# Optimization experiments

Measured on AMD Instinct MI355X. Metric: run time of the kernel, lower is better.

Reference implementation:

```python
import jax, jax.numpy as jnp
import numpy as np


def setup_inputs() -> dict:
    key = jax.random.key(0)
    k1, k2 = jax.random.split(key)
    src_map = jax.random.normal(k1, (8, 256, 48, 48), dtype=jnp.float32)
    dst_map = jax.random.normal(k2, (8, 256, 48, 48), dtype=jnp.float32)
    return {"src_map": src_map, "dst_map": dst_map}


def reference(src_map, dst_map):
    # src_map: [B, C, H, W] -> flatten spatial to S = H*W
    B, C, H, W = src_map.shape
    src_flat = src_map.reshape(B, C, H * W)                 # [B, C, S]
    # L2-normalize along channel dim (torch.norm default: 2-norm, no eps)
    src = src_flat / jnp.linalg.norm(src_flat, axis=1, keepdims=True)
    dst = dst_map / jnp.linalg.norm(dst_map, axis=1, keepdims=True)  # [B, C, Y, X]
    # cosine correlation volume: for each src pixel s, dot with every dst pixel
    gcm = jnp.einsum('bcs,bcyx->bsyx', src, dst)            # [B, S, Y, X]
    # torch.max(gcm, 0) == ReLU clamp
    return jnp.maximum(gcm, 0.0)
```

## Files before the change

### kernel.cpp

```cpp
#include <hip/hip_runtime.h>
#include <hip/hip_bf16.h>

#define B_DIM 8
#define C_DIM 256
#define S_DIM 2304

typedef __attribute__((ext_vector_type(8))) short short8;
typedef __attribute__((ext_vector_type(4))) float floatx4;

__device__ __forceinline__ void gload_lds16(const __hip_bfloat16* g, __hip_bfloat16* l) {
    __builtin_amdgcn_global_load_lds(
        (__attribute__((address_space(1))) void*)(void*)(g),
        (__attribute__((address_space(3))) void*)(l), 16, 0, 0);
}

__global__ __launch_bounds__(256) void norm_transpose_kernel(
    const float* __restrict__ src, const float* __restrict__ dst,
    __hip_bfloat16* __restrict__ srcT, __hip_bfloat16* __restrict__ dstT) {
    const int s0 = blockIdx.x * 64;
    const int b  = blockIdx.y;
    const float* in = (blockIdx.z == 0 ? src : dst) + (size_t)b * C_DIM * S_DIM;
    __hip_bfloat16* out = (blockIdx.z == 0 ? srcT : dstT) + (size_t)b * S_DIM * C_DIM;

    __shared__ __align__(16) __hip_bfloat16 tile[64][C_DIM + 8];
    __shared__ float red[4][64];
    __shared__ float invn[64];

    const int t  = threadIdx.x;
    const int l  = t & 63;
    const int wv = t >> 6;

    float ss = 0.f;
#pragma unroll 8
    for (int c = wv; c < C_DIM; c += 4) {
        float v = in[(size_t)c * S_DIM + s0 + l];
        ss += v * v;
        tile[l][c] = __float2bfloat16(v);
    }
    red[wv][l] = ss;
    __syncthreads();
    if (t < 64) invn[t] = rsqrtf(red[0][t] + red[1][t] + red[2][t] + red[3][t]);
    __syncthreads();

#pragma unroll
    for (int it = 0; it < 8; ++it) {
        int idx  = it * 256 + t;
        int srow = idx >> 5;
        int c0   = (idx & 31) << 3;
        float inv = invn[srow];
        union { short8 v; __hip_bfloat16 h[8]; } u, o;
        u.v = *(const short8*)&tile[srow][c0];
#pragma unroll
        for (int j = 0; j < 8; ++j)
            o.h[j] = __float2bfloat16(__bfloat162float(u.h[j]) * inv);
        *(short8*)&out[(size_t)(s0 + srow) * C_DIM + c0] = o.v;
    }
}

__global__ __launch_bounds__(256) void gemm_relu_kernel(
    const __hip_bfloat16* __restrict__ At, const __hip_bfloat16* __restrict__ Bt,
    float* __restrict__ out) {
    const int b  = blockIdx.z;
    const int m0 = blockIdx.y * 128;
    const int n0 = blockIdx.x * 128;
    const __hip_bfloat16* A  = At + (size_t)b * S_DIM * C_DIM;
    const __hip_bfloat16* Bp = Bt + (size_t)b * S_DIM * C_DIM;

    __shared__ __align__(16) __hip_bfloat16 As[128 * 32];
    __shared__ __align__(16) __hip_bfloat16 Bs[128 * 32];

    const int t    = threadIdx.x;
    const int lane = t & 63;
    const int wv   = t >> 6;

    const int fm = lane & 15;
    const int kq = (lane >> 4) << 3;
    const int wr = (wv >> 1) << 6;
    const int wc = (wv & 1) << 6;

    const int ch0 = wv * 2;

    floatx4 acc[4][4] = {};

    for (int k0 = 0; k0 < C_DIM; k0 += 32) {
#pragma unroll
        for (int ci = 0; ci < 2; ++ci) {
            int ch  = ch0 + ci;
            int e   = ch * 512 + lane * 8;
            int row = e >> 5;
            int kc  = e & 31;
            gload_lds16(A  + (size_t)(m0 + row) * C_DIM + (k0 + kc), &As[ch * 512]);
            gload_lds16(Bp + (size_t)(n0 + row) * C_DIM + (k0 + kc), &Bs[ch * 512]);
        }
        __syncthreads();

        short8 af[4], bf[4];
#pragma unroll
        for (int i = 0; i < 4; ++i) {
            af[i] = *(const short8*)&As[(wr + i * 16 + fm) * 32 + kq];
            bf[i] = *(const short8*)&Bs[(wc + i * 16 + fm) * 32 + kq];
        }
#pragma unroll
        for (int i = 0; i < 4; ++i)
#pragma unroll
            for (int j = 0; j < 4; ++j)
                acc[i][j] = __builtin_amdgcn_mfma_f32_16x16x32_bf16(af[i], bf[j], acc[i][j], 0, 0, 0);
        __syncthreads();
    }

    float* Cp = out + (size_t)b * S_DIM * S_DIM;
    const int rq = (lane >> 4) << 2;
#pragma unroll
    for (int i = 0; i < 4; ++i) {
        int rbase = m0 + wr + i * 16 + rq;
#pragma unroll
        for (int j = 0; j < 4; ++j) {
            int col = n0 + wc + j * 16 + fm;
#pragma unroll
            for (int r = 0; r < 4; ++r)
                Cp[(size_t)(rbase + r) * S_DIM + col] = fmaxf(acc[i][j][r], 0.f);
        }
    }
}

extern "C" void kernel_launch(void* const* d_in, const int* in_sizes, int n_in,
                              void* d_out, int out_size, void* d_ws, size_t ws_size,
                              hipStream_t stream) {
    const float* src = (const float*)d_in[0];
    const float* dst = (const float*)d_in[1];
    float* out = (float*)d_out;

    __hip_bfloat16* srcT = (__hip_bfloat16*)d_ws;
    __hip_bfloat16* dstT = srcT + (size_t)B_DIM * S_DIM * C_DIM;

    dim3 g1(S_DIM / 64, B_DIM, 2);
    norm_transpose_kernel<<<g1, 256, 0, stream>>>(src, dst, srcT, dstT);

    dim3 g2(S_DIM / 128, S_DIM / 128, B_DIM);
    gemm_relu_kernel<<<g2, 256, 0, stream>>>(srcT, dstT, out);
}
```

Before: 220.5 us.

## Double-buffer GEMM LDS tiles and stage epilogue through LDS for vector stores

The GEMM K-loop now double-buffers the A/B tiles in shared memory, prefetching the next K slice with global_load_lds while MFMAs run on the current one. This drops one barrier per iteration and overlaps load latency with compute. The ReLU epilogue writes accumulators into a padded LDS tile in two halves and then stores rows to global memory as coalesced float4, replacing scattered scalar stores. The cost is extra barriers in the epilogue and a larger shared-memory footprint (about 33 KB), which may reduce occupancy.

After: 221.8 us. Within noise of the previous version (+0.6%).

```diff
diff --git a/kernel.cpp b/kernel.cpp
--- a/kernel.cpp
+++ b/kernel.cpp
@@ -66,8 +66,9 @@
     const __hip_bfloat16* A  = At + (size_t)b * S_DIM * C_DIM;
     const __hip_bfloat16* Bp = Bt + (size_t)b * S_DIM * C_DIM;
 
-    __shared__ __align__(16) __hip_bfloat16 As[128 * 32];
-    __shared__ __align__(16) __hip_bfloat16 Bs[128 * 32];
+    __shared__ __align__(16) unsigned char smem[33792];
+    __hip_bfloat16* stg = (__hip_bfloat16*)smem;
+    float* Cs = (float*)smem;
 
     const int t    = threadIdx.x;
     const int lane = t & 63;
@@ -77,48 +78,78 @@
     const int kq = (lane >> 4) << 3;
     const int wr = (wv >> 1) << 6;
     const int wc = (wv & 1) << 6;
+    const int rq = (lane >> 4) << 2;
 
-    const int ch0 = wv * 2;
+    const int ch0   = wv * 2;
+    const int e0    = ch0 * 512 + lane * 8;
+    const int row0  = e0 >> 5;
+    const int kc0   = e0 & 31;
+    const int e1    = (ch0 + 1) * 512 + lane * 8;
+    const int row1  = e1 >> 5;
+    const int kc1   = e1 & 31;
 
     floatx4 acc[4][4] = {};
 
-    for (int k0 = 0; k0 < C_DIM; k0 += 32) {
+    {
+        gload_lds16(A  + (size_t)(m0 + row0) * C_DIM + kc0, stg + 0 * 4096 + ch0 * 512);
+        gload_lds16(A  + (size_t)(m0 + row1) * C_DIM + kc1, stg + 0 * 4096 + (ch0 + 1) * 512);
+        gload_lds16(Bp + (size_t)(n0 + row0) * C_DIM + kc0, stg + 8192 + 0 * 4096 + ch0 * 512);
+        gload_lds16(Bp + (size_t)(n0 + row1) * C_DIM + kc1, stg + 8192 + 0 * 4096 + (ch0 + 1) * 512);
+    }
+
 #pragma unroll
-        for (int ci = 0; ci < 2; ++ci) {
-            int ch  = ch0 + ci;
-            int e   = ch * 512 + lane * 8;
-            int row = e >> 5;
-            int kc  = e & 31;
-            gload_lds16(A  + (size_t)(m0 + row) * C_DIM + (k0 + kc), &As[ch * 512]);
-            gload_lds16(Bp + (size_t)(n0 + row) * C_DIM + (k0 + kc), &Bs[ch * 512]);
-        }
+    for (int ki = 0; ki < 8; ++ki) {
         __syncthreads();
 
+        if (ki < 7) {
+            int kn = (ki + 1) * 32;
+            int pb = (ki + 1) & 1;
+            gload_lds16(A  + (size_t)(m0 + row0) * C_DIM + (kn + kc0), stg + pb * 4096 + ch0 * 512);
+            gload_lds16(A  + (size_t)(m0 + row1) * C_DIM + (kn + kc1), stg + pb * 4096 + (ch0 + 1) * 512);
+            gload_lds16(Bp + (size_t)(n0 + row0) * C_DIM + (kn + kc0), stg + 8192 + pb * 4096 + ch0 * 512);
+            gload_lds16(Bp + (size_t)(n0 + row1) * C_DIM + (kn + kc1), stg + 8192 + pb * 4096 + (ch0 + 1) * 512);
+        }
+
+        const __hip_bfloat16* AsP = stg + (ki & 1) * 4096;
+        const __hip_bfloat16* BsP = stg + 8192 + (ki & 1) * 4096;
         short8 af[4], bf[4];
 #pragma unroll
         for (int i = 0; i < 4; ++i) {
-            af[i] = *(const short8*)&As[(wr + i * 16 + fm) * 32 + kq];
-            bf[i] = *(const short8*)&Bs[(wc + i * 16 + fm) * 32 + kq];
+            af[i] = *(const short8*)&AsP[(wr + i * 16 + fm) * 32 + kq];
+            bf[i] = *(const short8*)&BsP[(wc + i * 16 + fm) * 32 + kq];
         }
 #pragma unroll
         for (int i = 0; i < 4; ++i)
 #pragma unroll
             for (int j = 0; j < 4; ++j)
                 acc[i][j] = __builtin_amdgcn_mfma_f32_16x16x32_bf16(af[i], bf[j], acc[i][j], 0, 0, 0);
-        __syncthreads();
     }
 
     float* Cp = out + (size_t)b * S_DIM * S_DIM;
-    const int rq = (lane >> 4) << 2;
 #pragma unroll
-    for (int i = 0; i < 4; ++i) {
-        int rbase = m0 + wr + i * 16 + rq;
+    for (int p = 0; p < 2; ++p) {
+        __syncthreads();
 #pragma unroll
-        for (int j = 0; j < 4; ++j) {
-            int col = n0 + wc + j * 16 + fm;
+        for (int i2 = 0; i2 < 2; ++i2) {
+            int i = 2 * p + i2;
+            int slot = (wr >> 1) + i2 * 16 + rq;
 #pragma unroll
-            for (int r = 0; r < 4; ++r)
-                Cp[(size_t)(rbase + r) * S_DIM + col] = fmaxf(acc[i][j][r], 0.f);
+            for (int j = 0; j < 4; ++j) {
+                int col = wc + j * 16 + fm;
+#pragma unroll
+                for (int r = 0; r < 4; ++r)
+                    Cs[(slot + r) * 132 + col] = fmaxf(acc[i][j][r], 0.f);
+            }
+        }
+        __syncthreads();
+#pragma unroll
+        for (int it = 0; it < 8; ++it) {
+            int idx  = it * 256 + t;
+            int srow = idx >> 5;
+            int c4   = (idx & 31) << 2;
+            float4 v = *(const float4*)&Cs[srow * 132 + c4];
+            int lrow = 32 * p + (srow & 31) + ((srow >> 5) << 6);
+            *(float4*)&Cp[(size_t)(m0 + lrow) * S_DIM + n0 + c4] = v;
         }
     }
 }
```
